# Performance work log

Hardware: AMD Instinct MI355X
Metric: run time of the kernel (lower is better)

## Reference

```python
import jax, jax.numpy as jnp
import numpy as np

D = 768      # feature_dim
HD = 768     # hidden_dim
NH = 4       # num_heads
B, T1, T2 = 4, 128, 128
LN_EPS = 1e-5

def setup_inputs() -> dict:
    key = jax.random.key(0)
    ks = jax.random.split(key, 12)
    s = 0.02
    return {
        'speech_features': jax.random.normal(ks[0], (B, T1, D), jnp.float32),
        'phoneme_features': jax.random.normal(ks[1], (B, T2, D), jnp.float32),
        # per-head attention MLP: Linear(2D->HD), ReLU, Linear(HD->1); stacked over heads
        'W1': jax.random.normal(ks[2], (NH, 2 * D, HD), jnp.float32) * s,
        'b1': jnp.zeros((NH, HD), jnp.float32),
        'w2': jax.random.normal(ks[3], (NH, HD), jnp.float32) * s,
        'b2': jnp.zeros((NH,), jnp.float32),
        # fusion: Linear(2D->2HD), ReLU, Linear(2HD->D), LayerNorm(D)
        'Wf1': jax.random.normal(ks[4], (2 * D, 2 * HD), jnp.float32) * s,
        'bf1': jnp.zeros((2 * HD,), jnp.float32),
        'Wf2': jax.random.normal(ks[5], (2 * HD, D), jnp.float32) * s,
        'bf2': jnp.zeros((D,), jnp.float32),
        'ln_g': jnp.ones((D,), jnp.float32),
        'ln_b': jnp.zeros((D,), jnp.float32),
    }

def reference(speech_features, phoneme_features, W1, b1, w2, b2, Wf1, bf1, Wf2, bf2, ln_g, ln_b):
    d = speech_features.shape[-1]
    # Decompose Linear(cat([speech_t, phoneme])) = speech@W1[:d] + phoneme@W1[d:] + b1
    Wx, Wy = W1[:, :d, :], W1[:, d:, :]
    sx = jnp.einsum('btd,ndh->nbth', speech_features, Wx)   # [NH,B,T1,HD]
    py = jnp.einsum('bsd,ndh->nbsh', phoneme_features, Wy)  # [NH,B,T2,HD]
    hidden = jax.nn.relu(sx[:, :, :, None, :] + py[:, :, None, :, :]
                         + b1[:, None, None, None, :])      # [NH,B,T1,T2,HD]
    scores = jnp.einsum('nbtsh,nh->nbts', hidden, w2) + b2[:, None, None, None]
    attn = jax.nn.softmax(scores, axis=-1).mean(axis=0)     # [B,T1,T2]
    context = jnp.einsum('bts,bsd->btd', attn, phoneme_features)  # [B,T1,D]
    fused = jnp.concatenate([speech_features, context], axis=-1)  # [B,T1,2D]
    # dropout is identity in eval mode
    h = jax.nn.relu(fused @ Wf1 + bf1)
    out = h @ Wf2 + bf2
    mu = out.mean(axis=-1, keepdims=True)
    var = ((out - mu) ** 2).mean(axis=-1, keepdims=True)
    out = (out - mu) * jax.lax.rsqrt(var + LN_EPS) * ln_g + ln_b
    return out.mean(axis=1)  # [B,D]
```

## Files before the change

kernel.cpp:

```cpp
#include <hip/hip_runtime.h>
#include <cstddef>


#define D_  768
#define HD_ 768
#define NH_ 4
#define B_  4
#define T1_ 128
#define T2_ 128
#define M_  (B_*T1_)
#define LN_EPS_ 1e-5f

typedef unsigned short u16;
typedef unsigned int u32;
typedef _Float16 f16;
typedef _Float16 f16x2 __attribute__((ext_vector_type(2)));
typedef __bf16 bf16x8 __attribute__((ext_vector_type(8)));
typedef float f32x4 __attribute__((ext_vector_type(4)));

__device__ __forceinline__ u16 f2bf(float f) {
    union { float f; unsigned int u; } v; v.f = f;
    unsigned int u = v.u + (0x7FFFu + ((v.u >> 16) & 1u));
    return (u16)(u >> 16);
}
__device__ __forceinline__ u32 pack_bf2(float lo, float hi) {
    return (u32)f2bf(lo) | ((u32)f2bf(hi) << 16);
}
__device__ __forceinline__ u16 f16bits(f16 h) {
    return __builtin_bit_cast(unsigned short, h);
}
__device__ __forceinline__ f16x2 bcast2(u32 u) {
    return __builtin_bit_cast(f16x2, u);
}
__device__ __forceinline__ u32 splat2(u16 h) { return (u32)h * 0x10001u; }

template<bool RELU, int MODE, bool AF32>
__device__ __forceinline__ void gemm_mfma_body(
    const void* __restrict__ Av, int lda,
    const u16* __restrict__ Bt, int ldb,
    const float* __restrict__ bias,
    void* __restrict__ C, int ldc, int K, int m0, int n0)
{
    __shared__ __align__(16) u16 As[64][40];
    __shared__ __align__(16) u16 Bs[64][40];
    __shared__ u16 Ts[MODE == 3 ? 64 : 1][MODE == 3 ? 68 : 1];

    const int tid = threadIdx.x;
    const int row = tid >> 2;
    const int kq  = (tid & 3) << 3;
    const int lane = tid & 63;
    const int w  = tid >> 6;
    const int wr = (w >> 1) << 5;
    const int wc = (w & 1) << 5;
    const int l16 = lane & 15;
    const int lk8 = (lane >> 4) << 3;
    const int r4  = (lane >> 4) << 2;

    const u16*   aptr16 = (const u16*)Av + (size_t)(m0 + row) * lda + kq;
    const float* aptrf  = (const float*)Av + (size_t)(m0 + row) * lda + kq;
    const u16*   bptr   = Bt + (size_t)(n0 + row) * ldb + kq;

    f32x4 acc00 = {0.f,0.f,0.f,0.f}, acc01 = {0.f,0.f,0.f,0.f};
    f32x4 acc10 = {0.f,0.f,0.f,0.f}, acc11 = {0.f,0.f,0.f,0.f};

    auto loadA = [&](int k0) -> uint4 {
        if (AF32) {
            float4 ax = *(const float4*)(aptrf + k0);
            float4 ay = *(const float4*)(aptrf + k0 + 4);
            uint4 r;
            r.x = pack_bf2(ax.x, ax.y); r.y = pack_bf2(ax.z, ax.w);
            r.z = pack_bf2(ay.x, ay.y); r.w = pack_bf2(ay.z, ay.w);
            return r;
        }
        return *(const uint4*)(aptr16 + k0);
    };

    uint4 a_nxt = loadA(0);
    uint4 b_nxt = *(const uint4*)bptr;

    for (int k0 = 0; k0 < K; k0 += 32) {
        __syncthreads();
        *(uint4*)&As[row][kq] = a_nxt;
        *(uint4*)&Bs[row][kq] = b_nxt;
        if (k0 + 32 < K) {
            a_nxt = loadA(k0 + 32);
            b_nxt = *(const uint4*)(bptr + k0 + 32);
        }
        __syncthreads();
        bf16x8 af0 = *(const bf16x8*)&As[wr + l16][lk8];
        bf16x8 af1 = *(const bf16x8*)&As[wr + 16 + l16][lk8];
        bf16x8 bf0 = *(const bf16x8*)&Bs[wc + l16][lk8];
        bf16x8 bf1 = *(const bf16x8*)&Bs[wc + 16 + l16][lk8];
        acc00 = __builtin_amdgcn_mfma_f32_16x16x32_bf16(af0, bf0, acc00, 0, 0, 0);
        acc01 = __builtin_amdgcn_mfma_f32_16x16x32_bf16(af0, bf1, acc01, 0, 0, 0);
        acc10 = __builtin_amdgcn_mfma_f32_16x16x32_bf16(af1, bf0, acc10, 0, 0, 0);
        acc11 = __builtin_amdgcn_mfma_f32_16x16x32_bf16(af1, bf1, acc11, 0, 0, 0);
    }

#define EPI_FRAG(ACC, MF, NF)                                                  \
    {                                                                          \
        const int gcol = n0 + wc + (NF)*16 + l16;                              \
        const float bv = bias ? bias[gcol] : 0.f;                              \
        float v_[4];                                                           \
        _Pragma("unroll")                                                      \
        for (int r = 0; r < 4; r++) {                                          \
            float v = ACC[r] + bv;                                             \
            if (RELU) v = fmaxf(v, 0.f);                                       \
            v_[r] = v;                                                         \
        }                                                                      \
        const int lr0 = wr + (MF)*16 + r4;                                     \
        if (MODE == 3) {                                                       \
            const int lc = wc + (NF)*16 + l16;                                 \
            _Pragma("unroll")                                                  \
            for (int r = 0; r < 4; r++) Ts[lc][lr0 + r] = f16bits((f16)v_[r]); \
        } else {                                                               \
            _Pragma("unroll")                                                  \
            for (int r = 0; r < 4; r++) {                                      \
                const size_t off = (size_t)(m0 + lr0 + r) * ldc + gcol;        \
                if (MODE == 0) ((float*)C)[off] = v_[r];                       \
                else if (MODE == 1) ((u16*)C)[off] = f2bf(v_[r]);              \
                else ((u16*)C)[off] = f16bits((f16)v_[r]);                     \
            }                                                                  \
        }                                                                      \
    }
    EPI_FRAG(acc00, 0, 0) EPI_FRAG(acc01, 0, 1)
    EPI_FRAG(acc10, 1, 0) EPI_FRAG(acc11, 1, 1)
#undef EPI_FRAG

    if (MODE == 3) {
        __syncthreads();
        u16* cb = (u16*)C + (size_t)(m0 >> 7) * (768 * 128) + (m0 & 127);
#pragma unroll
        for (int u = 0; u < 4; u++) {
            const int i = tid + u * 256;
            const int hl = i >> 4;
            const int s4 = (i & 15) << 2;
            ushort4 o;
            o.x = Ts[hl][s4 + 0]; o.y = Ts[hl][s4 + 1];
            o.z = Ts[hl][s4 + 2]; o.w = Ts[hl][s4 + 3];
            *(ushort4*)(cb + (size_t)(n0 + hl) * 128 + s4) = o;
        }
    }
}

__global__ __launch_bounds__(256) void prep_kernel(
    const float* __restrict__ W1, const float* __restrict__ Wf1,
    const float* __restrict__ Wf2,
    u16* __restrict__ w1t, u16* __restrict__ wf1t, u16* __restrict__ wf2t)
{
    const int tid = threadIdx.x;
    int bid = blockIdx.x;
    const float* in; u16* outp; int tx, ty;
    if (bid < 4608) {
        const int z = bid / 1152, r = bid % 1152;
        tx = r % 24; ty = r / 24;
        in = W1 + (size_t)z * 1536 * 768; outp = w1t + (size_t)z * 768 * 1536;
    } else if (bid < 6912) {
        const int r = bid - 4608;
        tx = r % 48; ty = r / 48;
        in = Wf1; outp = wf1t;
    } else {
        const int r = bid - 6912;
        tx = r % 24; ty = r / 24;
        in = Wf2; outp = wf2t;
    }
    const int C = (bid >= 4608 && bid < 6912) ? 1536 : 768;
    const int c0 = tx * 32, r0 = ty * 32;
    __shared__ float tile[32][33];
    const int tr = tid >> 3, tc = (tid & 7) << 2;
    float4 v = *(const float4*)(in + (size_t)(r0 + tr) * C + c0 + tc);
    tile[tr][tc] = v.x; tile[tr][tc + 1] = v.y;
    tile[tr][tc + 2] = v.z; tile[tr][tc + 3] = v.w;
    __syncthreads();
    ushort4 o;
    o.x = f2bf(tile[tc + 0][tr]); o.y = f2bf(tile[tc + 1][tr]);
    o.z = f2bf(tile[tc + 2][tr]); o.w = f2bf(tile[tc + 3][tr]);
    *(ushort4*)(outp + (size_t)(c0 + tr) * 1536 + r0 + tc) = o;
}

__global__ __launch_bounds__(256) void gemm_sxpy_kernel(
    const float* __restrict__ sp, const float* __restrict__ ph,
    const u16* __restrict__ w1t, const float* __restrict__ b1,
    u16* __restrict__ sxf, u16* __restrict__ pyt)
{
    const int z = blockIdx.z;
    const int n = z & 3;
    const bool ispy = z >= 4;
    const u16* Bt = w1t + (size_t)n * 768 * 1536 + (ispy ? 768 : 0);
    if (!ispy) {
        gemm_mfma_body<false, 2, true>(sp, 768, Bt, 1536, b1 + n * HD_,
                                       sxf + (size_t)n * M_ * HD_, HD_, 768,
                                       blockIdx.y * 64, blockIdx.x * 64);
    } else {
        gemm_mfma_body<false, 3, true>(ph, 768, Bt, 1536, nullptr,
                                       pyt + (size_t)n * 4 * 768 * 128, 0, 768,
                                       blockIdx.y * 64, blockIdx.x * 64);
    }
}

template<bool RELU, int MODE>
__global__ __launch_bounds__(256) void gemm_mfma_kernel(
    const u16* __restrict__ A, int lda,
    const u16* __restrict__ Bt, int ldb,
    const float* __restrict__ bias,
    void* __restrict__ C, int ldc, int K)
{
    gemm_mfma_body<RELU, MODE, false>(A, lda, Bt, ldb, bias, C, ldc, K,
                                      blockIdx.y * 64, blockIdx.x * 64);
}

__global__ __launch_bounds__(512) void scores_ctx_kernel(
    const u16* __restrict__ sxf,
    const u16* __restrict__ pyt,
    const float* __restrict__ w2,
    const float* __restrict__ phon,
    const float* __restrict__ speech,
    u16* __restrict__ fused)
{
    const int bid = blockIdx.x;
    const int b = bid >> 6, t0 = (bid & 63) * 2;
    const int m0 = b * 128 + t0;
    const int tid = threadIdx.x, lane = tid & 63;
    const int W = tid >> 6;
    const int n = W >> 1, r = W & 1;

    __shared__ __align__(16) f16x2 sxs[4][2][768];
    __shared__ __align__(16) f16x2 w2s[4][768];
    __shared__ float attn4[4][2][128];
    __shared__ float attn[2][128];

#pragma unroll
    for (int q = 0; q < 3; q++) {
        const int u = lane + 64 * q;
        const int h4 = u * 4;
        ushort4 v = *(const ushort4*)(sxf + ((size_t)(n * 512 + m0 + r)) * 768 + h4);
        sxs[n][r][h4 + 0] = bcast2(splat2(v.x));
        sxs[n][r][h4 + 1] = bcast2(splat2(v.y));
        sxs[n][r][h4 + 2] = bcast2(splat2(v.z));
        sxs[n][r][h4 + 3] = bcast2(splat2(v.w));
        if (r == 0) {
            float4 wv = *(const float4*)(w2 + n * 768 + h4);
            w2s[n][h4 + 0] = bcast2(splat2(f16bits((f16)wv.x)));
            w2s[n][h4 + 1] = bcast2(splat2(f16bits((f16)wv.y)));
            w2s[n][h4 + 2] = bcast2(splat2(f16bits((f16)wv.z)));
            w2s[n][h4 + 3] = bcast2(splat2(f16bits((f16)wv.w)));
        }
    }
    __syncthreads();

    const f16x2* pypanel = (const f16x2*)(pyt + ((size_t)((n << 2) | b)) * 768 * 128) + lane;
    const f16x2 z2 = {(f16)0, (f16)0};

    float acc0 = 0.f, acc1 = 0.f;

    f16x2 b0[16], b1[16];
#pragma unroll
    for (int j = 0; j < 16; j++) b0[j] = pypanel[(size_t)j * 64];
#pragma unroll
    for (int j = 0; j < 16; j++) b1[j] = pypanel[(size_t)(16 + j) * 64];

    auto compute = [&](const f16x2 (&buf)[16], int hbase, f16x2 (&a4)[4]) {
#pragma unroll
        for (int j4 = 0; j4 < 16; j4 += 4) {
            uint4 sau = *(const uint4*)&sxs[n][r][hbase + j4];
            uint4 wvu = *(const uint4*)&w2s[n][hbase + j4];
            const u32 sa_[4] = {sau.x, sau.y, sau.z, sau.w};
            const u32 wv_[4] = {wvu.x, wvu.y, wvu.z, wvu.w};
#pragma unroll
            for (int j = 0; j < 4; j++) {
                f16x2 r_ = __builtin_elementwise_max(bcast2(sa_[j]) + buf[j4 + j], z2);
                a4[j] = __builtin_elementwise_fma(r_, bcast2(wv_[j]), a4[j]);
            }
        }
    };

    for (int hc = 0; hc < 768; hc += 32) {
        f16x2 a4[4] = {z2, z2, z2, z2};
        compute(b0, hc, a4);
        if (hc + 32 < 768) {
#pragma unroll
            for (int j = 0; j < 16; j++) b0[j] = pypanel[(size_t)(hc + 32 + j) * 64];
        }
        compute(b1, hc + 16, a4);
        if (hc + 48 < 768) {
#pragma unroll
            for (int j = 0; j < 16; j++) b1[j] = pypanel[(size_t)(hc + 48 + j) * 64];
        }
#pragma unroll
        for (int k = 0; k < 4; k++) {
            acc0 += (float)a4[k].x;
            acc1 += (float)a4[k].y;
        }
    }

    float mx = fmaxf(acc0, acc1);
#pragma unroll
    for (int off = 32; off; off >>= 1) mx = fmaxf(mx, __shfl_xor(mx, off, 64));
    const float e0 = expf(acc0 - mx), e1 = expf(acc1 - mx);
    float sm = e0 + e1;
#pragma unroll
    for (int off = 32; off; off >>= 1) sm += __shfl_xor(sm, off, 64);
    const float inv = 0.25f / sm;
    float2 pr; pr.x = e0 * inv; pr.y = e1 * inv;
    *(float2*)&attn4[n][r][2 * lane] = pr;
    __syncthreads();

    if (tid < 256) {
        const int rr = tid >> 7, s = tid & 127;
        attn[rr][s] = attn4[0][rr][s] + attn4[1][rr][s] + attn4[2][rr][s] + attn4[3][rr][s];
    }
    __syncthreads();

    {
        const int rr = tid >> 8;
        const int dbase = tid & 255;
        const int m = m0 + rr;
        const float* ph = phon + (size_t)b * 128 * 768;
#pragma unroll
        for (int j = 0; j < 3; j++) {
            const int d = dbase + 256 * j;
            float acc = 0.f;
#pragma unroll 8
            for (int s = 0; s < 128; s++)
                acc = fmaf(attn[rr][s], ph[(size_t)s * 768 + d], acc);
            fused[(size_t)m * 1536 + d] = f2bf(speech[(size_t)m * 768 + d]);
            fused[(size_t)m * 1536 + 768 + d] = f2bf(acc);
        }
    }
}

__global__ __launch_bounds__(256) void ln_fused_kernel(
    const float* __restrict__ x, const float* __restrict__ g,
    const float* __restrict__ lb, float* __restrict__ out)
{
    const int b = blockIdx.x / 3, c = blockIdx.x % 3;
    const int tid = threadIdx.x, lane = tid & 63, w = tid >> 6;
    __shared__ float rs[T1_];
    __shared__ float Sred[4];

    float prsum = 0.f;
    for (int i = 0; i < 32; i++) {
        const int row = w * 32 + i;
        const float4* x4 = (const float4*)(x + ((size_t)(b * T1_ + row)) * D_);
        float s = 0.f, ss = 0.f;
#pragma unroll
        for (int j = 0; j < 3; j++) {
            float4 v = x4[j * 64 + lane];
            s += v.x + v.y + v.z + v.w;
            ss += v.x * v.x + v.y * v.y + v.z * v.z + v.w * v.w;
        }
#pragma unroll
        for (int off = 32; off; off >>= 1) {
            s += __shfl_xor(s, off, 64);
            ss += __shfl_xor(ss, off, 64);
        }
        if (lane == 0) {
            const float mu = s * (1.f / D_);
            const float var = ss * (1.f / D_) - mu * mu;
            const float r = rsqrtf(var + LN_EPS_);
            rs[row] = r;
            prsum += mu * r;
        }
    }
    if (lane == 0) Sred[w] = prsum;
    __syncthreads();
    const float S = Sred[0] + Sred[1] + Sred[2] + Sred[3];
    const float* xb = x + (size_t)b * T1_ * D_;
    const int d = c * 256 + tid;
    float acc = 0.f;
#pragma unroll 8
    for (int t = 0; t < T1_; t++)
        acc = fmaf(xb[(size_t)t * D_ + d], rs[t], acc);
    out[b * D_ + d] = g[d] * (acc - S) * (1.f / T1_) + lb[d];
}

extern "C" void kernel_launch(void* const* d_in, const int* in_sizes, int n_in,
                              void* d_out, int out_size, void* d_ws, size_t ws_size,
                              hipStream_t stream)
{
    const float* speech = (const float*)d_in[0];
    const float* phon   = (const float*)d_in[1];
    const float* W1     = (const float*)d_in[2];
    const float* b1     = (const float*)d_in[3];
    const float* w2     = (const float*)d_in[4];
    const float* Wf1    = (const float*)d_in[6];
    const float* bf1    = (const float*)d_in[7];
    const float* Wf2    = (const float*)d_in[8];
    const float* bf2    = (const float*)d_in[9];
    const float* ln_g   = (const float*)d_in[10];
    const float* ln_b   = (const float*)d_in[11];
    float* out = (float*)d_out;

    char* w = (char*)d_ws;
    auto alloc = [&](size_t bytes) { char* p = w; w += (bytes + 1023) & ~(size_t)1023; return p; };
    u16* w1t    = (u16*)alloc((size_t)NH_ * 768 * 1536 * 2);
    u16* wf1t   = (u16*)alloc((size_t)1536 * 1536 * 2);
    u16* wf2t   = (u16*)alloc((size_t)768 * 1536 * 2);
    u16* sxf    = (u16*)alloc((size_t)NH_ * M_ * HD_ * 2);
    u16* pyt    = (u16*)alloc((size_t)NH_ * B_ * 768 * 128 * 2);
    u16* fusedb = (u16*)alloc((size_t)M_ * 2 * D_ * 2);
    u16* hbuf   = (u16*)alloc((size_t)M_ * 2 * HD_ * 2);
    float* outpre = (float*)alloc((size_t)M_ * D_ * 4);

    hipLaunchKernelGGL(prep_kernel, dim3(8064), dim3(256), 0, stream,
                       W1, Wf1, Wf2, w1t, wf1t, wf2t);
    hipLaunchKernelGGL(gemm_sxpy_kernel, dim3(HD_ / 64, M_ / 64, 8), dim3(256), 0, stream,
                       speech, phon, w1t, b1, sxf, pyt);
    hipLaunchKernelGGL(scores_ctx_kernel, dim3(256), dim3(512), 0, stream,
                       sxf, pyt, w2, phon, speech, fusedb);
    hipLaunchKernelGGL((gemm_mfma_kernel<true, 1>), dim3(2 * HD_ / 64, M_ / 64), dim3(256), 0, stream,
                       fusedb, 2 * D_, wf1t, 1536, bf1, hbuf, 2 * HD_, 2 * D_);
    hipLaunchKernelGGL((gemm_mfma_kernel<false, 0>), dim3(D_ / 64, M_ / 64), dim3(256), 0, stream,
                       hbuf, 2 * HD_, wf2t, 1536, bf2, outpre, D_, 2 * HD_);
    hipLaunchKernelGGL(ln_fused_kernel, dim3(12), dim3(256), 0, stream,
                       outpre, ln_g, ln_b, out);
}
```

Measured before the change: 128.5 us.

## Process both query rows per wave to reuse phoneme panel loads in scores kernel

The scores/context kernel drops from 512 to 256 threads. Each wave now handles both query rows for its head, so every loaded phoneme-projection value feeds two relu-fma chains and global panel traffic per row is halved. The context matvec likewise computes both rows from a single read of the phoneme features. The costs are half as many waves per block for hiding latency and more registers per thread. The __syncthreads after the shared-memory staging was removed, which looks safe because each wave reads only its own staged head slices.

```diff
diff --git a/kernel.cpp b/kernel.cpp
--- a/kernel.cpp
+++ b/kernel.cpp
@@ -209,7 +209,7 @@
                                       blockIdx.y * 64, blockIdx.x * 64);
 }
 
-__global__ __launch_bounds__(512) void scores_ctx_kernel(
+__global__ __launch_bounds__(256) void scores_ctx_kernel(
     const u16* __restrict__ sxf,
     const u16* __restrict__ pyt,
     const float* __restrict__ w2,
@@ -221,37 +221,38 @@
     const int b = bid >> 6, t0 = (bid & 63) * 2;
     const int m0 = b * 128 + t0;
     const int tid = threadIdx.x, lane = tid & 63;
-    const int W = tid >> 6;
-    const int n = W >> 1, r = W & 1;
+    const int n = tid >> 6;
 
     __shared__ __align__(16) f16x2 sxs[4][2][768];
     __shared__ __align__(16) f16x2 w2s[4][768];
     __shared__ float attn4[4][2][128];
-    __shared__ float attn[2][128];
-
+    __shared__ float2 attn[128];
+
+#pragma unroll
+    for (int r = 0; r < 2; r++)
+#pragma unroll
+        for (int q = 0; q < 3; q++) {
+            const int h4 = (lane + 64 * q) * 4;
+            ushort4 v = *(const ushort4*)(sxf + ((size_t)(n * 512 + m0 + r)) * 768 + h4);
+            sxs[n][r][h4 + 0] = bcast2(splat2(v.x));
+            sxs[n][r][h4 + 1] = bcast2(splat2(v.y));
+            sxs[n][r][h4 + 2] = bcast2(splat2(v.z));
+            sxs[n][r][h4 + 3] = bcast2(splat2(v.w));
+        }
 #pragma unroll
     for (int q = 0; q < 3; q++) {
-        const int u = lane + 64 * q;
-        const int h4 = u * 4;
-        ushort4 v = *(const ushort4*)(sxf + ((size_t)(n * 512 + m0 + r)) * 768 + h4);
-        sxs[n][r][h4 + 0] = bcast2(splat2(v.x));
-        sxs[n][r][h4 + 1] = bcast2(splat2(v.y));
-        sxs[n][r][h4 + 2] = bcast2(splat2(v.z));
-        sxs[n][r][h4 + 3] = bcast2(splat2(v.w));
-        if (r == 0) {
-            float4 wv = *(const float4*)(w2 + n * 768 + h4);
-            w2s[n][h4 + 0] = bcast2(splat2(f16bits((f16)wv.x)));
-            w2s[n][h4 + 1] = bcast2(splat2(f16bits((f16)wv.y)));
-            w2s[n][h4 + 2] = bcast2(splat2(f16bits((f16)wv.z)));
-            w2s[n][h4 + 3] = bcast2(splat2(f16bits((f16)wv.w)));
-        }
-    }
-    __syncthreads();
+        const int h4 = (lane + 64 * q) * 4;
+        float4 wv = *(const float4*)(w2 + n * 768 + h4);
+        w2s[n][h4 + 0] = bcast2(splat2(f16bits((f16)wv.x)));
+        w2s[n][h4 + 1] = bcast2(splat2(f16bits((f16)wv.y)));
+        w2s[n][h4 + 2] = bcast2(splat2(f16bits((f16)wv.z)));
+        w2s[n][h4 + 3] = bcast2(splat2(f16bits((f16)wv.w)));
+    }
 
     const f16x2* pypanel = (const f16x2*)(pyt + ((size_t)((n << 2) | b)) * 768 * 128) + lane;
     const f16x2 z2 = {(f16)0, (f16)0};
 
-    float acc0 = 0.f, acc1 = 0.f;
+    float accA0 = 0.f, accA1 = 0.f, accB0 = 0.f, accB1 = 0.f;
 
     f16x2 b0[16], b1[16];
 #pragma unroll
@@ -259,72 +260,96 @@
 #pragma unroll
     for (int j = 0; j < 16; j++) b1[j] = pypanel[(size_t)(16 + j) * 64];
 
-    auto compute = [&](const f16x2 (&buf)[16], int hbase, f16x2 (&a4)[4]) {
+    auto compute = [&](const f16x2 (&buf)[16], int hbase) {
+        f16x2 aA = z2, aB = z2;
 #pragma unroll
         for (int j4 = 0; j4 < 16; j4 += 4) {
-            uint4 sau = *(const uint4*)&sxs[n][r][hbase + j4];
+            uint4 sau = *(const uint4*)&sxs[n][0][hbase + j4];
+            uint4 sbu = *(const uint4*)&sxs[n][1][hbase + j4];
             uint4 wvu = *(const uint4*)&w2s[n][hbase + j4];
             const u32 sa_[4] = {sau.x, sau.y, sau.z, sau.w};
+            const u32 sb_[4] = {sbu.x, sbu.y, sbu.z, sbu.w};
             const u32 wv_[4] = {wvu.x, wvu.y, wvu.z, wvu.w};
 #pragma unroll
             for (int j = 0; j < 4; j++) {
-                f16x2 r_ = __builtin_elementwise_max(bcast2(sa_[j]) + buf[j4 + j], z2);
-                a4[j] = __builtin_elementwise_fma(r_, bcast2(wv_[j]), a4[j]);
+                const f16x2 pv = buf[j4 + j];
+                const f16x2 wj = bcast2(wv_[j]);
+                f16x2 ra = __builtin_elementwise_max(bcast2(sa_[j]) + pv, z2);
+                f16x2 rb = __builtin_elementwise_max(bcast2(sb_[j]) + pv, z2);
+                aA = __builtin_elementwise_fma(ra, wj, aA);
+                aB = __builtin_elementwise_fma(rb, wj, aB);
             }
         }
+        accA0 += (float)aA.x; accA1 += (float)aA.y;
+        accB0 += (float)aB.x; accB1 += (float)aB.y;
     };
 
     for (int hc = 0; hc < 768; hc += 32) {
-        f16x2 a4[4] = {z2, z2, z2, z2};
-        compute(b0, hc, a4);
+        compute(b0, hc);
         if (hc + 32 < 768) {
 #pragma unroll
             for (int j = 0; j < 16; j++) b0[j] = pypanel[(size_t)(hc + 32 + j) * 64];
         }
-        compute(b1, hc + 16, a4);
+        compute(b1, hc + 16);
         if (hc + 48 < 768) {
 #pragma unroll
             for (int j = 0; j < 16; j++) b1[j] = pypanel[(size_t)(hc + 48 + j) * 64];
         }
-#pragma unroll
-        for (int k = 0; k < 4; k++) {
-            acc0 += (float)a4[k].x;
-            acc1 += (float)a4[k].y;
-        }
-    }
-
-    float mx = fmaxf(acc0, acc1);
-#pragma unroll
-    for (int off = 32; off; off >>= 1) mx = fmaxf(mx, __shfl_xor(mx, off, 64));
-    const float e0 = expf(acc0 - mx), e1 = expf(acc1 - mx);
-    float sm = e0 + e1;
-#pragma unroll
-    for (int off = 32; off; off >>= 1) sm += __shfl_xor(sm, off, 64);
-    const float inv = 0.25f / sm;
-    float2 pr; pr.x = e0 * inv; pr.y = e1 * inv;
-    *(float2*)&attn4[n][r][2 * lane] = pr;
+    }
+
+#pragma unroll
+    for (int which = 0; which < 2; which++) {
+        const float s0 = which ? accB0 : accA0;
+        const float s1 = which ? accB1 : accA1;
+        float mx = fmaxf(s0, s1);
+#pragma unroll
+        for (int off = 32; off; off >>= 1) mx = fmaxf(mx, __shfl_xor(mx, off, 64));
+        const float e0 = expf(s0 - mx), e1 = expf(s1 - mx);
+        float sm = e0 + e1;
+#pragma unroll
+        for (int off = 32; off; off >>= 1) sm += __shfl_xor(sm, off, 64);
+        const float inv = 0.25f / sm;
+        float2 pr; pr.x = e0 * inv; pr.y = e1 * inv;
+        *(float2*)&attn4[n][which][2 * lane] = pr;
+    }
     __syncthreads();
 
-    if (tid < 256) {
-        const int rr = tid >> 7, s = tid & 127;
-        attn[rr][s] = attn4[0][rr][s] + attn4[1][rr][s] + attn4[2][rr][s] + attn4[3][rr][s];
+    if (tid < 128) {
+        const int s = tid;
+        float2 a;
+        a.x = attn4[0][0][s] + attn4[1][0][s] + attn4[2][0][s] + attn4[3][0][s];
+        a.y = attn4[0][1][s] + attn4[1][1][s] + attn4[2][1][s] + attn4[3][1][s];
+        attn[s] = a;
     }
     __syncthreads();
 
     {
-        const int rr = tid >> 8;
-        const int dbase = tid & 255;
-        const int m = m0 + rr;
         const float* ph = phon + (size_t)b * 128 * 768;
+        const int d0 = tid;
+        float acc0[3] = {0.f, 0.f, 0.f};
+        float acc1[3] = {0.f, 0.f, 0.f};
+        for (int s8 = 0; s8 < 128; s8 += 8) {
+            float2 at[8];
+#pragma unroll
+            for (int k = 0; k < 8; k++) at[k] = attn[s8 + k];
+#pragma unroll
+            for (int j = 0; j < 3; j++) {
+                const int d = d0 + 256 * j;
+#pragma unroll
+                for (int k = 0; k < 8; k++) {
+                    const float pv = ph[(size_t)(s8 + k) * 768 + d];
+                    acc0[j] = fmaf(at[k].x, pv, acc0[j]);
+                    acc1[j] = fmaf(at[k].y, pv, acc1[j]);
+                }
+            }
+        }
 #pragma unroll
         for (int j = 0; j < 3; j++) {
-            const int d = dbase + 256 * j;
-            float acc = 0.f;
-#pragma unroll 8
-            for (int s = 0; s < 128; s++)
-                acc = fmaf(attn[rr][s], ph[(size_t)s * 768 + d], acc);
-            fused[(size_t)m * 1536 + d] = f2bf(speech[(size_t)m * 768 + d]);
-            fused[(size_t)m * 1536 + 768 + d] = f2bf(acc);
+            const int d = d0 + 256 * j;
+            fused[(size_t)m0 * 1536 + d] = f2bf(speech[(size_t)m0 * 768 + d]);
+            fused[(size_t)m0 * 1536 + 768 + d] = f2bf(acc0[j]);
+            fused[(size_t)(m0 + 1) * 1536 + d] = f2bf(speech[(size_t)(m0 + 1) * 768 + d]);
+            fused[(size_t)(m0 + 1) * 1536 + 768 + d] = f2bf(acc1[j]);
         }
     }
 }
@@ -406,7 +431,7 @@
                        W1, Wf1, Wf2, w1t, wf1t, wf2t);
     hipLaunchKernelGGL(gemm_sxpy_kernel, dim3(HD_ / 64, M_ / 64, 8), dim3(256), 0, stream,
                        speech, phon, w1t, b1, sxf, pyt);
-    hipLaunchKernelGGL(scores_ctx_kernel, dim3(256), dim3(512), 0, stream,
+    hipLaunchKernelGGL(scores_ctx_kernel, dim3(256), dim3(256), 0, stream,
                        sxf, pyt, w2, phon, speech, fusedb);
     hipLaunchKernelGGL((gemm_mfma_kernel<true, 1>), dim3(2 * HD_ / 64, M_ / 64), dim3(256), 0, stream,
                        fusedb, 2 * D_, wf1t, 1536, bf1, hbuf, 2 * HD_, 2 * D_);
```

Measured after the change: 114.8 us. -10.7%, faster.
